# Kernel tuning notes

Measured on AMD Instinct MI355X. Metric: run time of the kernel, lower is better.

Reference implementation:

```python
import jax, jax.numpy as jnp
import numpy as np

N = 100_000   # nodes
E = 3_200_000 # directed edges (avg degree 32)
D = 256       # feature dim (in_channels)
K = 2         # k of k-MIS


def _propagate_min(min_rank, row, col, n, k):
    # k iterations of scatter_min along edges (row -> col), keeping current value
    for _ in range(k):
        neigh = jax.ops.segment_min(min_rank[row], col, num_segments=n)
        min_rank = jnp.minimum(min_rank, neigh)
    return min_rank


def maximal_k_independent_set(row, col, rank, n, k):
    # Luby-style greedy k-MIS: repeatedly add nodes whose rank is minimal in their
    # k-hop in-neighbourhood, then mark (cover) the k-hop neighbourhood of the MIS.
    def dilate(mask):
        for _ in range(k):
            neigh = jax.ops.segment_max(mask[row].astype(jnp.int32), col, num_segments=n)
            mask = mask | (neigh > 0)
        return mask

    def cond(state):
        _, mask, _ = state
        return ~jnp.all(mask)

    def body(state):
        mis, mask, min_rank = state
        min_rank = _propagate_min(min_rank, row, col, n, k)
        mis = mis | (rank == min_rank)
        mask = dilate(mis)
        min_rank = jnp.where(mask, n, rank)  # covered nodes get rank 'infinity' (= n)
        return mis, mask, min_rank

    z = jnp.zeros((n,), dtype=bool)
    mis, _, _ = jax.lax.while_loop(cond, body, (z, z, rank))
    return mis


def cluster_k_mis(mis, row, col, rank, n, k):
    # min_rank = n everywhere except MIS nodes get their rank; propagate min k hops;
    # cluster id = index of the unique MIS rank each node ends up attached to.
    min_rank = jnp.where(mis, rank, n)
    min_rank = _propagate_min(min_rank, row, col, n, k)
    _, clusters = jnp.unique(min_rank, return_inverse=True)
    return clusters.reshape(-1).astype(jnp.int32)


def setup_inputs():
    key = jax.random.key(0)
    k1, k2, k3 = jax.random.split(key, 3)
    x = jax.random.normal(k1, (N, D), dtype=jnp.float32)
    edge_index = jax.random.randint(k2, (2, E), 0, N, dtype=jnp.int32)
    edge_attr = jax.random.normal(k3, (E,), dtype=jnp.float32)
    return {"x": x, "edge_index": edge_index, "edge_attr": edge_attr}


def reference(x, edge_index, edge_attr):
    n = x.shape[0]
    row, col = edge_index[0], edge_index[1]
    # scorer=None -> score = arange(n); greedy ordering of arange -> rank = arange(n)
    rank = jnp.arange(n, dtype=jnp.int32)

    mis = maximal_k_independent_set(row, col, rank, n, K)
    cluster = cluster_k_mis(mis, row, col, rank, n, K)
    c = int(mis.sum())  # number of clusters (MIS size)

    # --- pooled adjacency: coalesce duplicate (cluster[row], cluster[col]) with sum ---
    cl_np = np.asarray(cluster).astype(np.int64)
    r = cl_np[np.asarray(row)]
    cc = cl_np[np.asarray(col)]
    keys = r * np.int64(c) + cc
    uniq, inv = np.unique(keys, return_inverse=True)
    val = jax.ops.segment_sum(edge_attr, jnp.asarray(inv.astype(np.int32)),
                              num_segments=int(uniq.shape[0]))
    new_row = (uniq // c).astype(np.int32)
    new_col = (uniq % c).astype(np.int32)
    keep = np.nonzero(new_row != new_col)[0]  # remove_self_loops=True
    pooled_edge_index = jnp.stack([jnp.asarray(new_row[keep]), jnp.asarray(new_col[keep])])
    pooled_edge_attr = val[jnp.asarray(keep)]

    # --- pooled node features: reduce_x='sum' (adaptive=False, so no score scaling) ---
    x_pooled = jax.ops.segment_sum(x, cluster, num_segments=c)
    return x_pooled, pooled_edge_index, pooled_edge_attr
```

## Files before the change

### kernel.cpp

```cpp
#include <hip/hip_runtime.h>
#include <cmath>
#include <cstdint>

#define NT 256
#define EG0 1024
#define EG1 256
#define MAX_ROUND 16
#define SCAN_T 32
#define SCAN_IPB (NT*SCAN_T)


__device__ __forceinline__ int block_append(int* cursor, bool pred, int* s_w){
  int wid  = threadIdx.x >> 6;
  int lane = threadIdx.x & 63;
  unsigned long long m = __ballot(pred);
  int cnt = __popcll(m);
  if(lane==0) s_w[wid]=cnt;
  __syncthreads();
  if(threadIdx.x==0){
    int t0=s_w[0], t1=s_w[1], t2=s_w[2], t3=s_w[3];
    int tot=t0+t1+t2+t3;
    int base = tot ? atomicAdd(cursor, tot) : 0;
    s_w[0]=base; s_w[1]=base+t0; s_w[2]=base+t0+t1; s_w[3]=base+t0+t1+t2;
  }
  __syncthreads();
  int pos = s_w[wid] + __popcll(m & ((1ull<<lane)-1ull));
  __syncthreads();
  return pos;
}


__global__ void k_init(int* a, int* b, int n){
  int v = blockIdx.x*NT + threadIdx.x;
  if(v<n){ a[v]=v; b[v]=v; }
}


__global__ void k_hop0(int* b, const int* __restrict__ row,
                       const int* __restrict__ col, int E){
  int stride = gridDim.x*NT;
  for(int e = blockIdx.x*NT + threadIdx.x; e<E; e+=stride){
    int s = row[e];
    if(s < b[col[e]]) atomicMin(&b[col[e]], s);
  }
}

__global__ void k_hop0f(int* a, const int* b, const int* __restrict__ row,
                        const int* __restrict__ col, int n, int E){
  int stride = gridDim.x*NT;
  int total = n + E;
  for(int i = blockIdx.x*NT + threadIdx.x; i<total; i+=stride){
    if(i<n){
      if(b[i] < a[i]) atomicMin(&a[i], b[i]);
    } else {
      int e = i-n;
      int s = b[row[e]];
      if(s < a[col[e]]) atomicMin(&a[col[e]], s);
    }
  }
}

__global__ void k_dil0(const int* a, int* d2, int* cover, const int* __restrict__ row,
                       const int* __restrict__ col, int E, int ep){
  int stride = gridDim.x*NT;
  for(int e = blockIdx.x*NT + threadIdx.x; e<E; e+=stride){
    int r = row[e];
    if(a[r]==r){
      int cc = col[e];
      d2[r]=ep;  cover[r]=1;
      d2[cc]=ep; cover[cc]=1;
    }
  }
}

__global__ void k_dil20(const int* a, const int* d2, int* cover, const int* __restrict__ row,
                        const int* __restrict__ col, int E, int ep){
  int stride = gridDim.x*NT;
  for(int e = blockIdx.x*NT + threadIdx.x; e<E; e+=stride){
    int r = row[e];
    if((d2[r]==ep || a[r]==r) && !cover[col[e]]) cover[col[e]]=1;
  }
}

__global__ void k_fincomp0(int* a, int* b, int* mis, int* cover, int n,
                           const int* __restrict__ row, const int* __restrict__ col, int E,
                           int2* Ld, int* lcnt1, int* U1, int* rcnt0){
  __shared__ int s_w[4];
  long nth = (long)gridDim.x*NT;
  for(long base = (long)blockIdx.x*NT; base < n; base += nth){
    int v = (int)base + threadIdx.x;
    bool unc = false;
    if(v<n){
      int nw = (a[v]==v);
      if(nw){ mis[v]=1; if(!cover[v]) cover[v]=1; }
      int cov = cover[v] | nw;
      int val = cov ? n : v;
      a[v]=val; b[v]=val;
      unc = !cov;
    }
    int pos = block_append(rcnt0, unc, s_w);
    if(unc) U1[pos]=v;
  }
  for(long base = (long)blockIdx.x*NT; base < E; base += nth){
    int e = (int)base + threadIdx.x;
    bool keep=false; int2 ed;
    if(e<E){
      ed = make_int2(row[e], col[e]);
      keep = (!cover[ed.x]) || (!cover[ed.y]);
    }
    int pos = block_append(lcnt1, keep, s_w);
    if(keep) Ld[pos]=ed;
  }
}


__global__ void k_hop1(int* b, const int* a, const int2* L, const int* pE,
                       const int* gate){
  if(*gate==0) return;
  int E = *pE;
  int stride = gridDim.x*NT;
  for(int e = blockIdx.x*NT + threadIdx.x; e<E; e+=stride){
    int2 ed = L[e];
    int s = a[ed.x];
    if(s < b[ed.y]) atomicMin(&b[ed.y], s);
  }
}

__global__ void k_hop1f(int* a, const int* b, const int2* L, const int* pE,
                        const int* U, const int* pU, const int* gate){
  if(*gate==0) return;
  int E = *pE, un = *pU;
  int total = un + E;
  int stride = gridDim.x*NT;
  for(int i = blockIdx.x*NT + threadIdx.x; i<total; i+=stride){
    if(i<un){
      int u = U[i];
      if(b[u] < a[u]) atomicMin(&a[u], b[u]);
    } else {
      int2 ed = L[i-un];
      int s = b[ed.x];
      if(s < a[ed.y]) atomicMin(&a[ed.y], s);
    }
  }
}

__global__ void k_dil11(const int* a, int* d2, int* cover, int* mis, const int2* L,
                        const int* pE, const int* U, const int* pU, const int* gate, int ep){
  if(*gate==0) return;
  int E = *pE, un = *pU;
  int total = un + E;
  int stride = gridDim.x*NT;
  for(int i = blockIdx.x*NT + threadIdx.x; i<total; i+=stride){
    if(i<un){
      int u = U[i];
      if(a[u]==u){ mis[u]=1; cover[u]=1; d2[u]=ep; }
    } else {
      int2 ed = L[i-un];
      if(a[ed.x]==ed.x){ d2[ed.x]=ep; cover[ed.x]=1; d2[ed.y]=ep; cover[ed.y]=1; }
    }
  }
}

__global__ void k_dil21(const int* a, const int* d2, int* cover, const int2* L,
                        const int* pE, const int* gate, int ep){
  if(*gate==0) return;
  int E = *pE;
  int stride = gridDim.x*NT;
  for(int e = blockIdx.x*NT + threadIdx.x; e<E; e+=stride){
    int2 ed = L[e];
    if((d2[ed.x]==ep || a[ed.x]==ed.x) && !cover[ed.y]) cover[ed.y]=1;
  }
}

__global__ void k_fincomp1(int* a, int* b, const int* cover, int n,
                           const int2* Ls, const int* pE, int2* Ld, int* lcntD,
                           const int* Us, const int* pU, int* Ud, int* rcntD,
                           const int* gate){
  if(*gate==0) return;
  __shared__ int s_w[4];
  int E = *pE, un = *pU;
  long nth = (long)gridDim.x*NT;
  for(long base = (long)blockIdx.x*NT; base < un; base += nth){
    int i = (int)base + threadIdx.x;
    bool unc=false; int u=0;
    if(i<un){ u = Us[i]; unc = !cover[u]; }
    int pos = block_append(rcntD, unc, s_w);
    if(unc) Ud[pos]=u;
  }
  for(long base = (long)blockIdx.x*NT; base < E; base += nth){
    int e = (int)base + threadIdx.x;
    bool keep=false; int2 ed;
    if(e<E){
      ed = Ls[e];
      int vx = cover[ed.x] ? n : ed.x;  a[ed.x]=vx; b[ed.x]=vx;
      int vy = cover[ed.y] ? n : ed.y;  a[ed.y]=vy; b[ed.y]=vy;
      keep = (!cover[ed.x]) || (!cover[ed.y]);
    }
    int pos = block_append(lcntD, keep, s_w);
    if(keep) Ld[pos]=ed;
  }
}


__global__ void k_cluster_init(const int* mis, int* a, int* b, int n){
  int v = blockIdx.x*NT + threadIdx.x;
  if(v<n){ int m = mis[v] ? v : n; a[v]=m; b[v]=m; }
}

__global__ void k_chop1(int* b, const int* a, const int* __restrict__ row,
                        const int* __restrict__ col, int n, int E){
  int stride = gridDim.x*NT;
  for(int e = blockIdx.x*NT + threadIdx.x; e<E; e+=stride){
    int s = a[row[e]];
    if(s < n && s < b[col[e]]) atomicMin(&b[col[e]], s);
  }
}

__global__ void k_chop2f(int* a, const int* b, const int* __restrict__ row,
                         const int* __restrict__ col, int n, int E){
  int stride = gridDim.x*NT;
  int total = n + E;
  for(int i = blockIdx.x*NT + threadIdx.x; i<total; i+=stride){
    if(i<n){
      if(b[i] < a[i]) atomicMin(&a[i], b[i]);
    } else {
      int e = i-n;
      int s = b[row[e]];
      if(s < n && s < a[col[e]]) atomicMin(&a[col[e]], s);
    }
  }
}

__global__ void k_mark(const int* mr, const int* mis, int* present, int* cmis, int n){
  int v = blockIdx.x*NT + threadIdx.x;
  int m = 0;
  if(v<n){
    int r = mr[v];
    if(r<n) present[r]=1;
    m = mis[v];
  }
  __shared__ int sh[NT];
  sh[threadIdx.x]=m; __syncthreads();
  for(int off=NT/2; off>0; off>>=1){
    if(threadIdx.x<off) sh[threadIdx.x]+=sh[threadIdx.x+off];
    __syncthreads();
  }
  if(threadIdx.x==0 && sh[0]) atomicAdd(cmis, sh[0]);
}


__global__ void k_scan1(const int* A, int M, int* bsum){
  int t = threadIdx.x;
  long base = (long)blockIdx.x*SCAN_IPB + (long)t*SCAN_T;
  int s = 0;
  #pragma unroll
  for(int j=0;j<SCAN_T;j++){ long i=base+j; if(i<M) s += A[i]; }
  __shared__ int sh[NT];
  sh[t]=s; __syncthreads();
  for(int off=NT/2; off>0; off>>=1){ if(t<off) sh[t]+=sh[t+off]; __syncthreads(); }
  if(t==0) bsum[blockIdx.x]=sh[0];
}

__global__ void k_scan2(const int* bsum, int* bscan, int B, int* totalOut){
  __shared__ int sh[NT];
  int t = threadIdx.x;
  int carry = 0;
  for(int base=0; base<B; base+=NT){
    int i = base+t;
    int v = (i<B) ? bsum[i] : 0;
    sh[t]=v; __syncthreads();
    for(int off=1; off<NT; off<<=1){
      int x=0; if(t>=off) x=sh[t-off];
      __syncthreads();
      sh[t]+=x; __syncthreads();
    }
    int incl = sh[t];
    if(i<B) bscan[i] = carry + incl - v;
    carry += sh[NT-1];
    __syncthreads();
  }
  if(t==0 && totalOut) *totalOut = carry;
}

__global__ void k_scan3(const int* A, int M, const int* bscan, int* pref){
  int t = threadIdx.x;
  long base = (long)blockIdx.x*SCAN_IPB + (long)t*SCAN_T;
  int s = 0;
  #pragma unroll
  for(int j=0;j<SCAN_T;j++){ long i=base+j; if(i<M) s += A[i]; }
  __shared__ int sh[NT];
  sh[t]=s; __syncthreads();
  for(int off=1; off<NT; off<<=1){
    int x=0; if(t>=off) x=sh[t-off];
    __syncthreads();
    sh[t]+=x; __syncthreads();
  }
  int run = bscan[blockIdx.x] + (sh[t]-s);
  for(int j=0;j<SCAN_T;j++){
    long i=base+j;
    if(i<M){ pref[i]=run; run += A[i]; }
  }
}


__global__ void k_assign(const int* mr, const int* pref, int* cl, int* ccount, int n){
  int v = blockIdx.x*NT + threadIdx.x;
  if(v<n){
    int r = mr[v];
    int cid = (r<n) ? pref[r] : 0;
    cl[v]=cid;
    atomicAdd(&ccount[cid],1);
  }
}

__global__ void k_scatter_nodes(const int* cl, const int* cstart, int* cursor, int* nodeList, int n){
  int v = blockIdx.x*NT + threadIdx.x;
  if(v<n){
    int cid = cl[v];
    int pos = cstart[cid] + atomicAdd(&cursor[cid],1);
    nodeList[pos]=v;
  }
}

__global__ void k_pool_x(const float* __restrict__ x, const int* nodeList, const int* cstart,
                         const int* ccount, const int* scal, float* out, long out_size){
  int c = scal[0], U = scal[1];
  int t = threadIdx.x;
  for(int cid=blockIdx.x; cid<c; cid+=gridDim.x){
    float s = 0.f, s2 = 0.f;
    if(cid<U){
      int st = cstart[cid], cn = ccount[cid];
      int i=0;
      for(; i+1<cn; i+=2){
        int nd0 = nodeList[st+i], nd1 = nodeList[st+i+1];
        s  += x[(size_t)nd0*256 + t];
        s2 += x[(size_t)nd1*256 + t];
      }
      if(i<cn) s += x[(size_t)nodeList[st+i]*256 + t];
      s += s2;
    }
    long idx = (long)cid*256 + t;
    if(idx < out_size) out[idx]=s;
  }
}

__global__ void k_edge_pool(const int* __restrict__ row, const int* __restrict__ col,
                            const float* __restrict__ attr, const int* cl,
                            const int* scal, float* dense, unsigned int* bits, int E, long CMsq){
  int c = scal[0];
  int stride = gridDim.x*NT;
  for(int e = blockIdx.x*NT + threadIdx.x; e<E; e+=stride){
    long key = (long)cl[row[e]]*c + cl[col[e]];
    if(key < CMsq){
      atomicAdd(&dense[key], attr[e]);
      unsigned int msk = 1u<<((int)key&31);
      if(!(bits[key>>5] & msk)) atomicOr(&bits[key>>5], msk);
    }
  }
}

__global__ void k_cscan1(const unsigned int* bits, const int* scal, int* bsum, long CMsq){
  int c = scal[0];
  long M = (long)c*c; if(M>CMsq) M=CMsq;
  int t = threadIdx.x;
  long base = (long)blockIdx.x*SCAN_IPB + (long)t*SCAN_T;
  int s = 0;
  if(base < M && c > 0){
    int r = (int)(base / c);
    int q = (int)(base - (long)r*c);
    for(int j=0;j<SCAN_T;j++){
      long i=base+j;
      if(i<M){
        if(((bits[i>>5]>>((int)i&31))&1u) && r!=q) s++;
      }
      if(++q==c){ q=0; r++; }
    }
  }
  __shared__ int sh[NT];
  sh[t]=s; __syncthreads();
  for(int off=NT/2; off>0; off>>=1){ if(t<off) sh[t]+=sh[t+off]; __syncthreads(); }
  if(t==0) bsum[blockIdx.x]=sh[0];
}

__global__ void k_cemit(const unsigned int* bits, const float* dense, const int* scal,
                        const int* bscan, float* out, long out_size, long CMsq){
  int c = scal[0]; int P = scal[2];
  long M = (long)c*c; if(M>CMsq) M=CMsq;
  long xoff = (long)c*256;
  int t = threadIdx.x;
  long base = (long)blockIdx.x*SCAN_IPB + (long)t*SCAN_T;
  int s = 0;
  int r0=0,q0=0;
  if(base < M && c > 0){
    r0 = (int)(base / c);
    q0 = (int)(base - (long)r0*c);
    int r=r0, q=q0;
    for(int j=0;j<SCAN_T;j++){
      long i=base+j;
      if(i<M){
        if(((bits[i>>5]>>((int)i&31))&1u) && r!=q) s++;
      }
      if(++q==c){ q=0; r++; }
    }
  }
  __shared__ int sh[NT];
  sh[t]=s; __syncthreads();
  for(int off=1; off<NT; off<<=1){
    int x=0; if(t>=off) x=sh[t-off];
    __syncthreads();
    sh[t]+=x; __syncthreads();
  }
  int run = bscan[blockIdx.x] + (sh[t]-s);
  if(base < M && c > 0){
    int r=r0, q=q0;
    for(int j=0;j<SCAN_T;j++){
      long i=base+j;
      if(i<M && ((bits[i>>5]>>((int)i&31))&1u) && r!=q){
        long o0 = xoff + run;
        long o1 = xoff + (long)P + run;
        long o2 = xoff + 2L*(long)P + run;
        if(o0<out_size) out[o0]=(float)r;
        if(o1<out_size) out[o1]=(float)q;
        if(o2<out_size) out[o2]=dense[i];
        run++;
      }
      if(++q==c){ q=0; r++; }
    }
  }
}


extern "C" void kernel_launch(void* const* d_in, const int* in_sizes, int n_in,
                              void* d_out, int out_size, void* d_ws, size_t ws_size,
                              hipStream_t stream){
  (void)n_in;
  const float* x     = (const float*)d_in[0];
  const int*   eidx  = (const int*)d_in[1];
  const float* eattr = (const float*)d_in[2];
  const int D = 256;
  int n = in_sizes[0]/D;
  int E = in_sizes[1]/2;
  const int* row = eidx;
  const int* col = eidx + E;

  char* p = (char*)d_ws;
  auto alloc = [&](size_t bytes)->char*{ char* r=p; p += (bytes+255)&~(size_t)255; return r; };
  int2* LA   = (int2*)alloc((size_t)E*8);
  int2* LB   = (int2*)alloc((size_t)E*8);
  int* a     = (int*)alloc((size_t)n*4);
  int* b     = (int*)alloc((size_t)n*4);
  int* cl    = (int*)alloc((size_t)n*4);
  int* nodeList = (int*)alloc((size_t)n*4);
  int* pref  = (int*)alloc((size_t)n*4);
  int* U1    = (int*)alloc((size_t)n*4);
  int* U2    = (int*)alloc((size_t)n*4);
  int* bsum  = (int*)alloc(4096*4);
  int* bscan = (int*)alloc(4096*4);
  char* zstart = p;
  int* mis     = (int*)alloc((size_t)n*4);
  int* cover   = (int*)alloc((size_t)n*4);
  int* d2      = (int*)alloc((size_t)n*4);
  int* present = (int*)alloc((size_t)n*4);
  int* ccount  = (int*)alloc((size_t)n*4);
  int* cursor  = (int*)alloc((size_t)n*4);
  int* rcnt    = (int*)alloc((MAX_ROUND+2)*4);
  int* lcnt    = (int*)alloc((MAX_ROUND+2)*4);
  int* scal    = (int*)alloc(64);

  size_t used   = (size_t)(p-(char*)d_ws);
  size_t remain = (ws_size > used+4096) ? ws_size-used-4096 : 0;
  size_t cells  = remain/5;
  long CM = (long)std::sqrt((double)cells);
  while(CM>1 && CM*CM > (long)cells) CM--;
  if(CM>4096) CM=4096;
  if(CM<1) CM=1;
  long CMsq = CM*CM;
  unsigned int* bits = (unsigned int*)alloc(((size_t)CMsq/32 + 2)*4);
  float* dense       = (float*)alloc((size_t)CMsq*4);
  size_t zbytes = (size_t)(p - zstart);
  hipMemsetAsync(zstart, 0, zbytes, stream);

  int NB  = (n+NT-1)/NT;
  int NBs = (n+SCAN_IPB-1)/SCAN_IPB;
  int CB  = (int)((CMsq+SCAN_IPB-1)/SCAN_IPB);

  k_init    <<<NB,NT,0,stream>>>(a,b,n);
  k_hop0    <<<EG0,NT,0,stream>>>(b,row,col,E);
  k_hop0f   <<<EG0,NT,0,stream>>>(a,b,row,col,n,E);
  k_dil0    <<<EG0,NT,0,stream>>>(a,d2,cover,row,col,E,1);
  k_dil20   <<<EG0,NT,0,stream>>>(a,d2,cover,row,col,E,1);
  k_fincomp0<<<EG0,NT,0,stream>>>(a,b,mis,cover,n,row,col,E,LB,&lcnt[1],U1,&rcnt[0]);

  for(int r=1; r<MAX_ROUND; ++r){
    int2* Ls = (r&1) ? LB : LA;
    int2* Ld = (r&1) ? LA : LB;
    int*  Us = (r&1) ? U1 : U2;
    int*  Ud = (r&1) ? U2 : U1;
    int ep = r+1;
    k_hop1    <<<EG1,NT,0,stream>>>(b,a,Ls,&lcnt[r],&rcnt[r-1]);
    k_hop1f   <<<EG1,NT,0,stream>>>(a,b,Ls,&lcnt[r],Us,&rcnt[r-1],&rcnt[r-1]);
    k_dil11   <<<EG1,NT,0,stream>>>(a,d2,cover,mis,Ls,&lcnt[r],Us,&rcnt[r-1],&rcnt[r-1],ep);
    k_dil21   <<<EG1,NT,0,stream>>>(a,d2,cover,Ls,&lcnt[r],&rcnt[r-1],ep);
    k_fincomp1<<<EG1,NT,0,stream>>>(a,b,cover,n,Ls,&lcnt[r],Ld,&lcnt[r+1],
                                    Us,&rcnt[r-1],Ud,&rcnt[r],&rcnt[r-1]);
  }

  k_cluster_init<<<NB,NT,0,stream>>>(mis,a,b,n);
  k_chop1 <<<EG0,NT,0,stream>>>(b,a,row,col,n,E);
  k_chop2f<<<EG0,NT,0,stream>>>(a,b,row,col,n,E);

  k_mark <<<NB,NT,0,stream>>>(a,mis,present,scal,n);
  k_scan1<<<NBs,NT,0,stream>>>(present,n,bsum);
  k_scan2<<<1,NT,0,stream>>>(bsum,bscan,NBs,scal+1);
  k_scan3<<<NBs,NT,0,stream>>>(present,n,bscan,pref);
  k_assign<<<NB,NT,0,stream>>>(a,pref,cl,ccount,n);

  k_scan1<<<NBs,NT,0,stream>>>(ccount,n,bsum);
  k_scan2<<<1,NT,0,stream>>>(bsum,bscan,NBs,nullptr);
  k_scan3<<<NBs,NT,0,stream>>>(ccount,n,bscan,pref);
  k_scatter_nodes<<<NB,NT,0,stream>>>(cl,pref,cursor,nodeList,n);

  k_pool_x<<<512,NT,0,stream>>>(x,nodeList,pref,ccount,scal,(float*)d_out,(long)out_size);

  k_edge_pool<<<EG0,NT,0,stream>>>(row,col,eattr,cl,scal,dense,bits,E,CMsq);
  k_cscan1<<<CB,NT,0,stream>>>(bits,scal,bsum,CMsq);
  k_scan2 <<<1,NT,0,stream>>>(bsum,bscan,CB,scal+2);
  k_cemit <<<CB,NT,0,stream>>>(bits,dense,scal,bscan,(float*)d_out,(long)out_size,CMsq);
}
```

Measured before the change: 2.053 ms.

## Fuse second dilation hop with edge-list compaction and tune pooling launch

Merges the second dilation hop into the edge-compaction pass, in both the first round and the iterative rounds. This removes one full pass over the edge list per round. Node rank reset now sweeps all n nodes each round instead of writing through edge endpoints. Separately it doubles the iterative-round grid size, unrolls the feature-pooling sum by four, doubles its grid, and switches the dense edge accumulation to unsafeAtomicAdd. The fused compaction reads cover flags while other threads are still setting them, so some already-covered edges may survive one more round; this is conservative and keeps results correct.

Measured after the change: 2.232 ms. 8.7% more time.

```diff
diff --git a/kernel.cpp b/kernel.cpp
--- a/kernel.cpp
+++ b/kernel.cpp
@@ -4,7 +4,7 @@
 
 #define NT 256
 #define EG0 1024
-#define EG1 256
+#define EG1 512
 #define MAX_ROUND 16
 #define SCAN_T 32
 #define SCAN_IPB (NT*SCAN_T)
@@ -73,43 +73,43 @@
   }
 }
 
-__global__ void k_dil20(const int* a, const int* d2, int* cover, const int* __restrict__ row,
-                        const int* __restrict__ col, int E, int ep){
-  int stride = gridDim.x*NT;
-  for(int e = blockIdx.x*NT + threadIdx.x; e<E; e+=stride){
-    int r = row[e];
-    if((d2[r]==ep || a[r]==r) && !cover[col[e]]) cover[col[e]]=1;
-  }
-}
-
-__global__ void k_fincomp0(int* a, int* b, int* mis, int* cover, int n,
-                           const int* __restrict__ row, const int* __restrict__ col, int E,
-                           int2* Ld, int* lcnt1, int* U1, int* rcnt0){
+__global__ void k_dil20c(const int* a, const int* d2, int* cover,
+                         const int* __restrict__ row, const int* __restrict__ col,
+                         int E, int ep, int2* Ld, int* lcnt1){
   __shared__ int s_w[4];
   long nth = (long)gridDim.x*NT;
-  for(long base = (long)blockIdx.x*NT; base < n; base += nth){
+  for(long base=(long)blockIdx.x*NT; base<E; base+=nth){
+    int e=(int)base+threadIdx.x;
+    bool keep=false; int2 ed;
+    if(e<E){
+      ed = make_int2(row[e], col[e]);
+      int cx = cover[ed.x];
+      if((d2[ed.x]==ep || a[ed.x]==ed.x) && !cover[ed.y]) cover[ed.y]=1;
+      int cy = cover[ed.y];
+      keep = (!cx) || (!cy);
+    }
+    int pos = block_append(lcnt1, keep, s_w);
+    if(keep) Ld[pos]=ed;
+  }
+}
+
+__global__ void k_finnode0(int* a, int* b, int* mis, int* cover, int n,
+                           int* U1, int* rcnt0){
+  __shared__ int s_w[4];
+  long nth = (long)gridDim.x*NT;
+  for(long base=(long)blockIdx.x*NT; base<n; base+=nth){
     int v = (int)base + threadIdx.x;
-    bool unc = false;
+    bool unc=false;
     if(v<n){
       int nw = (a[v]==v);
+      int cov = cover[v] | nw;
       if(nw){ mis[v]=1; if(!cover[v]) cover[v]=1; }
-      int cov = cover[v] | nw;
       int val = cov ? n : v;
       a[v]=val; b[v]=val;
       unc = !cov;
     }
     int pos = block_append(rcnt0, unc, s_w);
     if(unc) U1[pos]=v;
-  }
-  for(long base = (long)blockIdx.x*NT; base < E; base += nth){
-    int e = (int)base + threadIdx.x;
-    bool keep=false; int2 ed;
-    if(e<E){
-      ed = make_int2(row[e], col[e]);
-      keep = (!cover[ed.x]) || (!cover[ed.y]);
-    }
-    int pos = block_append(lcnt1, keep, s_w);
-    if(keep) Ld[pos]=ed;
   }
 }
 
@@ -161,43 +161,46 @@
   }
 }
 
-__global__ void k_dil21(const int* a, const int* d2, int* cover, const int2* L,
-                        const int* pE, const int* gate, int ep){
+__global__ void k_dil21c(const int* a, const int* d2, int* cover,
+                         const int2* Ls, const int* pE, int ep,
+                         int2* Ld, int* lcntD, const int* gate){
   if(*gate==0) return;
+  __shared__ int s_w[4];
   int E = *pE;
-  int stride = gridDim.x*NT;
-  for(int e = blockIdx.x*NT + threadIdx.x; e<E; e+=stride){
-    int2 ed = L[e];
-    if((d2[ed.x]==ep || a[ed.x]==ed.x) && !cover[ed.y]) cover[ed.y]=1;
-  }
-}
-
-__global__ void k_fincomp1(int* a, int* b, const int* cover, int n,
-                           const int2* Ls, const int* pE, int2* Ld, int* lcntD,
+  long nth = (long)gridDim.x*NT;
+  for(long base=(long)blockIdx.x*NT; base<E; base+=nth){
+    int e=(int)base+threadIdx.x;
+    bool keep=false; int2 ed;
+    if(e<E){
+      ed = Ls[e];
+      int cx = cover[ed.x];
+      if((d2[ed.x]==ep || a[ed.x]==ed.x) && !cover[ed.y]) cover[ed.y]=1;
+      int cy = cover[ed.y];
+      keep = (!cx) || (!cy);
+    }
+    int pos = block_append(lcntD, keep, s_w);
+    if(keep) Ld[pos]=ed;
+  }
+}
+
+__global__ void k_finnode1(int* a, int* b, const int* cover, int n,
                            const int* Us, const int* pU, int* Ud, int* rcntD,
                            const int* gate){
   if(*gate==0) return;
   __shared__ int s_w[4];
-  int E = *pE, un = *pU;
   long nth = (long)gridDim.x*NT;
-  for(long base = (long)blockIdx.x*NT; base < un; base += nth){
-    int i = (int)base + threadIdx.x;
+  int stride = gridDim.x*NT;
+  for(int v = blockIdx.x*NT + threadIdx.x; v<n; v+=stride){
+    int val = cover[v] ? n : v;
+    a[v]=val; b[v]=val;
+  }
+  int un = *pU;
+  for(long base=(long)blockIdx.x*NT; base<un; base+=nth){
+    int i=(int)base+threadIdx.x;
     bool unc=false; int u=0;
-    if(i<un){ u = Us[i]; unc = !cover[u]; }
+    if(i<un){ u=Us[i]; unc = !cover[u]; }
     int pos = block_append(rcntD, unc, s_w);
     if(unc) Ud[pos]=u;
-  }
-  for(long base = (long)blockIdx.x*NT; base < E; base += nth){
-    int e = (int)base + threadIdx.x;
-    bool keep=false; int2 ed;
-    if(e<E){
-      ed = Ls[e];
-      int vx = cover[ed.x] ? n : ed.x;  a[ed.x]=vx; b[ed.x]=vx;
-      int vy = cover[ed.y] ? n : ed.y;  a[ed.y]=vy; b[ed.y]=vy;
-      keep = (!cover[ed.x]) || (!cover[ed.y]);
-    }
-    int pos = block_append(lcntD, keep, s_w);
-    if(keep) Ld[pos]=ed;
   }
 }
 
@@ -327,20 +330,22 @@
   int c = scal[0], U = scal[1];
   int t = threadIdx.x;
   for(int cid=blockIdx.x; cid<c; cid+=gridDim.x){
-    float s = 0.f, s2 = 0.f;
+    float s0=0.f, s1=0.f, s2=0.f, s3=0.f;
     if(cid<U){
       int st = cstart[cid], cn = ccount[cid];
       int i=0;
-      for(; i+1<cn; i+=2){
-        int nd0 = nodeList[st+i], nd1 = nodeList[st+i+1];
-        s  += x[(size_t)nd0*256 + t];
-        s2 += x[(size_t)nd1*256 + t];
+      for(; i+3<cn; i+=4){
+        int n0=nodeList[st+i], n1=nodeList[st+i+1], n2=nodeList[st+i+2], n3=nodeList[st+i+3];
+        s0 += x[(size_t)n0*256 + t];
+        s1 += x[(size_t)n1*256 + t];
+        s2 += x[(size_t)n2*256 + t];
+        s3 += x[(size_t)n3*256 + t];
       }
-      if(i<cn) s += x[(size_t)nodeList[st+i]*256 + t];
-      s += s2;
+      for(; i<cn; i++) s0 += x[(size_t)nodeList[st+i]*256 + t];
+      s0 += s1+s2+s3;
     }
     long idx = (long)cid*256 + t;
-    if(idx < out_size) out[idx]=s;
+    if(idx < out_size) out[idx]=s0;
   }
 }
 
@@ -352,7 +357,7 @@
   for(int e = blockIdx.x*NT + threadIdx.x; e<E; e+=stride){
     long key = (long)cl[row[e]]*c + cl[col[e]];
     if(key < CMsq){
-      atomicAdd(&dense[key], attr[e]);
+      unsafeAtomicAdd(&dense[key], attr[e]);
       unsigned int msk = 1u<<((int)key&31);
       if(!(bits[key>>5] & msk)) atomicOr(&bits[key>>5], msk);
     }
@@ -488,8 +493,8 @@
   k_hop0    <<<EG0,NT,0,stream>>>(b,row,col,E);
   k_hop0f   <<<EG0,NT,0,stream>>>(a,b,row,col,n,E);
   k_dil0    <<<EG0,NT,0,stream>>>(a,d2,cover,row,col,E,1);
-  k_dil20   <<<EG0,NT,0,stream>>>(a,d2,cover,row,col,E,1);
-  k_fincomp0<<<EG0,NT,0,stream>>>(a,b,mis,cover,n,row,col,E,LB,&lcnt[1],U1,&rcnt[0]);
+  k_dil20c  <<<EG0,NT,0,stream>>>(a,d2,cover,row,col,E,1,LB,&lcnt[1]);
+  k_finnode0<<<EG0,NT,0,stream>>>(a,b,mis,cover,n,U1,&rcnt[0]);
 
   for(int r=1; r<MAX_ROUND; ++r){
     int2* Ls = (r&1) ? LB : LA;
@@ -500,9 +505,8 @@
     k_hop1    <<<EG1,NT,0,stream>>>(b,a,Ls,&lcnt[r],&rcnt[r-1]);
     k_hop1f   <<<EG1,NT,0,stream>>>(a,b,Ls,&lcnt[r],Us,&rcnt[r-1],&rcnt[r-1]);
     k_dil11   <<<EG1,NT,0,stream>>>(a,d2,cover,mis,Ls,&lcnt[r],Us,&rcnt[r-1],&rcnt[r-1],ep);
-    k_dil21   <<<EG1,NT,0,stream>>>(a,d2,cover,Ls,&lcnt[r],&rcnt[r-1],ep);
-    k_fincomp1<<<EG1,NT,0,stream>>>(a,b,cover,n,Ls,&lcnt[r],Ld,&lcnt[r+1],
-                                    Us,&rcnt[r-1],Ud,&rcnt[r],&rcnt[r-1]);
+    k_dil21c  <<<EG1,NT,0,stream>>>(a,d2,cover,Ls,&lcnt[r],ep,Ld,&lcnt[r+1],&rcnt[r-1]);
+    k_finnode1<<<EG1,NT,0,stream>>>(a,b,cover,n,Us,&rcnt[r-1],Ud,&rcnt[r],&rcnt[r-1]);
   }
 
   k_cluster_init<<<NB,NT,0,stream>>>(mis,a,b,n);
@@ -520,7 +524,7 @@
   k_scan3<<<NBs,NT,0,stream>>>(ccount,n,bscan,pref);
   k_scatter_nodes<<<NB,NT,0,stream>>>(cl,pref,cursor,nodeList,n);
 
-  k_pool_x<<<512,NT,0,stream>>>(x,nodeList,pref,ccount,scal,(float*)d_out,(long)out_size);
+  k_pool_x<<<1024,NT,0,stream>>>(x,nodeList,pref,ccount,scal,(float*)d_out,(long)out_size);
 
   k_edge_pool<<<EG0,NT,0,stream>>>(row,col,eattr,cl,scal,dense,bits,E,CMsq);
   k_cscan1<<<CB,NT,0,stream>>>(bits,scal,bsum,CMsq);
```
